# Kernel optimization log

Measured on AMD Instinct MI355X. Metric: run time of the kernel, lower is better.

## Reference

```python
import jax, jax.numpy as jnp
import numpy as np

EPS = 1e-08

def _compute_W(V, C, eps=EPS):
    # W = H_k ... H_1, applied sequentially as in the torch loop
    W = jnp.eye(C, dtype=V.dtype)
    def step(W, v):
        v = v / (jnp.linalg.norm(v) + eps)
        # H @ W = W - 2 v (v^T W)
        W = W - 2.0 * jnp.outer(v, v @ W)
        return W, None
    W, _ = jax.lax.scan(step, W, V)
    return W

def setup_inputs() -> dict:
    key = jax.random.key(0)
    k1, k2 = jax.random.split(key)
    x = jax.random.normal(k1, (16, 512, 64, 64), dtype=jnp.float32)
    V = jax.random.normal(k2, (32, 512), dtype=jnp.float32)
    return {"x": x, "V": V}

def reference(x, V):
    B, C, H, Wd = x.shape
    W = _compute_W(V, C)  # [C, C] orthogonal
    # 1x1 conv: out[b,o,h,w] = sum_c W[o,c] * x[b,c,h,w]
    return jnp.einsum('oc,bchw->bohw', W, x)
```

## Files before the change

### kernel.cpp

```cpp
#include <hip/hip_runtime.h>
#include <hip/hip_bf16.h>
#include <stdint.h>
#include <stddef.h>

#define HH_EPS 1e-8f

typedef __attribute__((ext_vector_type(8))) short short8;
typedef __attribute__((ext_vector_type(4))) float f32x4;

__global__ void normalize_v(const float* __restrict__ V, float* __restrict__ vhat) {
    const int k = blockIdx.x;
    const int lane = threadIdx.x;
    const float4* row = (const float4*)(V + (size_t)k * 512);
    float4 a = row[lane * 2 + 0];
    float4 b = row[lane * 2 + 1];
    float ss = a.x*a.x + a.y*a.y + a.z*a.z + a.w*a.w
             + b.x*b.x + b.y*b.y + b.z*b.z + b.w*b.w;
    #pragma unroll
    for (int off = 32; off > 0; off >>= 1) ss += __shfl_xor(ss, off);
    const float inv = 1.0f / (sqrtf(ss) + HH_EPS);
    float4* orow = (float4*)(vhat + (size_t)k * 512);
    orow[lane * 2 + 0] = make_float4(a.x*inv, a.y*inv, a.z*inv, a.w*inv);
    orow[lane * 2 + 1] = make_float4(b.x*inv, b.y*inv, b.z*inv, b.w*inv);
}

__global__ void compute_w(const float* __restrict__ vhat,
                          __hip_bfloat16* __restrict__ Wb) {
    const int wave = threadIdx.x >> 6;
    const int lane = threadIdx.x & 63;
    const int j = blockIdx.x * 4 + wave;
    const int ib = lane * 8;

    float w[8];
    #pragma unroll
    for (int r = 0; r < 8; r++) w[r] = (ib + r == j) ? 1.0f : 0.0f;

    for (int k = 0; k < 32; k++) {
        const float4* vp = (const float4*)(vhat + (size_t)k * 512 + ib);
        float4 v0 = vp[0], v1 = vp[1];
        float v[8] = {v0.x, v0.y, v0.z, v0.w, v1.x, v1.y, v1.z, v1.w};
        float d = 0.0f;
        #pragma unroll
        for (int r = 0; r < 8; r++) d += v[r] * w[r];
        #pragma unroll
        for (int off = 32; off > 0; off >>= 1) d += __shfl_xor(d, off);
        const float t = 2.0f * d;
        #pragma unroll
        for (int r = 0; r < 8; r++) w[r] -= t * v[r];
    }
    #pragma unroll
    for (int r = 0; r < 8; r++)
        Wb[(size_t)(ib + r) * 512 + j] = __float2bfloat16(w[r]);
}

#define BM 128
#define BN 128
#define BK 32
#define CDIM 512
#define SDIM 4096
#define BROW 40

__global__ __launch_bounds__(256, 2) void hh_gemm(
    const float* __restrict__ x,
    const __hip_bfloat16* __restrict__ Wb,
    float* __restrict__ out)
{
    __shared__ __attribute__((aligned(16))) __hip_bfloat16 Alds[BM * BK];
    __shared__ __attribute__((aligned(16))) __hip_bfloat16 Blds[BN * BROW];

    const int tid  = threadIdx.x;
    const int wave = tid >> 6, lane = tid & 63;
    const int quad = lane >> 4, l16 = lane & 15;
    const int wm = wave >> 1, wn = wave & 1;

    const int mt = blockIdx.x;
    const int nt = blockIdx.y;
    const int b  = blockIdx.z;
    const int m0 = mt * BM, n0 = nt * BN;

    const float* xb = x + (size_t)b * CDIM * SDIM;

    f32x4 acc[4][4];
    #pragma unroll
    for (int i = 0; i < 4; i++)
        #pragma unroll
        for (int jj = 0; jj < 4; jj++) {
            f32x4 z = {0.0f, 0.0f, 0.0f, 0.0f};
            acc[i][jj] = z;
        }

    for (int kt = 0; kt < CDIM / BK; kt++) {
        const int k0 = kt * BK;
        __syncthreads();

        #pragma unroll
        for (int c = 0; c < 2; c++) {
            const int chunk = c * 256 + tid;
            const int row = chunk >> 2, seg = chunk & 3;
            const short8 av = *(const short8*)(Wb + (size_t)(m0 + row) * CDIM + k0 + seg * 8);
            *(short8*)(&Alds[chunk * 8]) = av;
        }

        #pragma unroll
        for (int c = 0; c < 2; c++) {
            const int u = c * 256 + tid;
            const int n = u & 127, kg = u >> 7;
            const float* gp = xb + (size_t)(k0 + kg * 8) * SDIM + n0 + n;
            float f[8];
            #pragma unroll
            for (int jj = 0; jj < 8; jj++) f[jj] = gp[(size_t)jj * SDIM];
            short8 pk;
            #pragma unroll
            for (int jj = 0; jj < 8; jj++) {
                __hip_bfloat16 h = __float2bfloat16(f[jj]);
                pk[jj] = *(short*)&h;
            }
            *(short8*)(&Blds[n * BROW + kg * 8]) = pk;
        }
        __syncthreads();

        short8 af[4], bfr[4];
        #pragma unroll
        for (int mi = 0; mi < 4; mi++)
            af[mi] = *(const short8*)(&Alds[(wm * 64 + mi * 16 + l16) * BK + quad * 8]);
        #pragma unroll
        for (int ni = 0; ni < 4; ni++)
            bfr[ni] = *(const short8*)(&Blds[(wn * 64 + ni * 16 + l16) * BROW + quad * 8]);
        #pragma unroll
        for (int mi = 0; mi < 4; mi++)
            #pragma unroll
            for (int ni = 0; ni < 4; ni++)
                acc[mi][ni] = __builtin_amdgcn_mfma_f32_16x16x32_bf16(
                    af[mi], bfr[ni], acc[mi][ni], 0, 0, 0);
    }

    float* ob = out + (size_t)b * CDIM * SDIM;
    #pragma unroll
    for (int mi = 0; mi < 4; mi++) {
        #pragma unroll
        for (int ni = 0; ni < 4; ni++) {
            const int col = n0 + wn * 64 + ni * 16 + l16;
            #pragma unroll
            for (int r = 0; r < 4; r++) {
                const int row = m0 + wm * 64 + mi * 16 + quad * 4 + r;
                ob[(size_t)row * SDIM + col] = acc[mi][ni][r];
            }
        }
    }
}

extern "C" void kernel_launch(void* const* d_in, const int* in_sizes, int n_in,
                              void* d_out, int out_size, void* d_ws, size_t ws_size,
                              hipStream_t stream) {
    const float* x = (const float*)d_in[0];
    const float* V = (const float*)d_in[1];
    float* out = (float*)d_out;

    float* vhat = (float*)d_ws;
    __hip_bfloat16* Wb = (__hip_bfloat16*)((char*)d_ws + 65536);

    normalize_v<<<32, 64, 0, stream>>>(V, vhat);
    compute_w<<<128, 256, 0, stream>>>(vhat, Wb);
    dim3 grid(4, 32, 16);
    hh_gemm<<<grid, 256, 0, stream>>>(x, Wb, out);
}
```

Measured before the change: 287.6 us.

## Double-buffer GEMM tiles, fuse normalization into W build, remap grid

Folds the V normalization into compute_w: the squared norm is reduced alongside the dot products, and each wave now handles two columns of W, which removes one kernel launch and the vhat round trip. The GEMM gets double-buffered LDS with register prefetch of the next K tile, so global loads overlap the MFMA work and there is one barrier per iteration. It also uses a 1D grid ordered so consecutive blocks share the same M tile, and raises launch bounds to 3 blocks per CU. The costs are higher register and LDS use per block and a possible occupancy shortfall if the compiler cannot fit three blocks.

```diff
diff --git a/kernel.cpp b/kernel.cpp
--- a/kernel.cpp
+++ b/kernel.cpp
@@ -8,49 +8,57 @@
 typedef __attribute__((ext_vector_type(8))) short short8;
 typedef __attribute__((ext_vector_type(4))) float f32x4;
 
-__global__ void normalize_v(const float* __restrict__ V, float* __restrict__ vhat) {
-    const int k = blockIdx.x;
-    const int lane = threadIdx.x;
-    const float4* row = (const float4*)(V + (size_t)k * 512);
-    float4 a = row[lane * 2 + 0];
-    float4 b = row[lane * 2 + 1];
-    float ss = a.x*a.x + a.y*a.y + a.z*a.z + a.w*a.w
-             + b.x*b.x + b.y*b.y + b.z*b.z + b.w*b.w;
-    #pragma unroll
-    for (int off = 32; off > 0; off >>= 1) ss += __shfl_xor(ss, off);
-    const float inv = 1.0f / (sqrtf(ss) + HH_EPS);
-    float4* orow = (float4*)(vhat + (size_t)k * 512);
-    orow[lane * 2 + 0] = make_float4(a.x*inv, a.y*inv, a.z*inv, a.w*inv);
-    orow[lane * 2 + 1] = make_float4(b.x*inv, b.y*inv, b.z*inv, b.w*inv);
-}
-
-__global__ void compute_w(const float* __restrict__ vhat,
+__global__ void compute_w(const float* __restrict__ V,
                           __hip_bfloat16* __restrict__ Wb) {
     const int wave = threadIdx.x >> 6;
     const int lane = threadIdx.x & 63;
-    const int j = blockIdx.x * 4 + wave;
+    const int jA = (blockIdx.x * 4 + wave) * 2;
+    const int jB = jA + 1;
     const int ib = lane * 8;
 
-    float w[8];
-    #pragma unroll
-    for (int r = 0; r < 8; r++) w[r] = (ib + r == j) ? 1.0f : 0.0f;
+    float wA[8], wB[8];
+    #pragma unroll
+    for (int r = 0; r < 8; r++) {
+        wA[r] = (ib + r == jA) ? 1.0f : 0.0f;
+        wB[r] = (ib + r == jB) ? 1.0f : 0.0f;
+    }
+
+    float4 c0 = *(const float4*)(V + ib);
+    float4 c1 = *(const float4*)(V + ib + 4);
 
     for (int k = 0; k < 32; k++) {
-        const float4* vp = (const float4*)(vhat + (size_t)k * 512 + ib);
-        float4 v0 = vp[0], v1 = vp[1];
-        float v[8] = {v0.x, v0.y, v0.z, v0.w, v1.x, v1.y, v1.z, v1.w};
-        float d = 0.0f;
-        #pragma unroll
-        for (int r = 0; r < 8; r++) d += v[r] * w[r];
-        #pragma unroll
-        for (int off = 32; off > 0; off >>= 1) d += __shfl_xor(d, off);
-        const float t = 2.0f * d;
-        #pragma unroll
-        for (int r = 0; r < 8; r++) w[r] -= t * v[r];
-    }
-    #pragma unroll
-    for (int r = 0; r < 8; r++)
-        Wb[(size_t)(ib + r) * 512 + j] = __float2bfloat16(w[r]);
+        const float v[8] = {c0.x, c0.y, c0.z, c0.w, c1.x, c1.y, c1.z, c1.w};
+        if (k < 31) {
+            c0 = *(const float4*)(V + (size_t)(k + 1) * 512 + ib);
+            c1 = *(const float4*)(V + (size_t)(k + 1) * 512 + ib + 4);
+        }
+        float dA = 0.0f, dB = 0.0f, ss = 0.0f;
+        #pragma unroll
+        for (int r = 0; r < 8; r++) {
+            dA += v[r] * wA[r];
+            dB += v[r] * wB[r];
+            ss += v[r] * v[r];
+        }
+        #pragma unroll
+        for (int off = 32; off > 0; off >>= 1) {
+            dA += __shfl_xor(dA, off);
+            dB += __shfl_xor(dB, off);
+            ss += __shfl_xor(ss, off);
+        }
+        const float t = sqrtf(ss) + HH_EPS;
+        const float scale = 2.0f / (t * t);
+        const float tA = scale * dA, tB = scale * dB;
+        #pragma unroll
+        for (int r = 0; r < 8; r++) {
+            wA[r] -= tA * v[r];
+            wB[r] -= tB * v[r];
+        }
+    }
+    #pragma unroll
+    for (int r = 0; r < 8; r++) {
+        Wb[(size_t)(ib + r) * 512 + jA] = __float2bfloat16(wA[r]);
+        Wb[(size_t)(ib + r) * 512 + jB] = __float2bfloat16(wB[r]);
+    }
 }
 
 #define BM 128
@@ -60,22 +68,67 @@
 #define SDIM 4096
 #define BROW 40
 
-__global__ __launch_bounds__(256, 2) void hh_gemm(
+__device__ __forceinline__ void issue_loads(
+    const float* __restrict__ xb, const __hip_bfloat16* __restrict__ Wb,
+    int k0, int m0, int n0, int tid, short8 a_pf[2], float b_pf[16])
+{
+    #pragma unroll
+    for (int c = 0; c < 2; c++) {
+        const int chunk = c * 256 + tid;
+        const int row = chunk >> 2, seg = chunk & 3;
+        a_pf[c] = *(const short8*)(Wb + (size_t)(m0 + row) * CDIM + k0 + seg * 8);
+    }
+    #pragma unroll
+    for (int c = 0; c < 2; c++) {
+        const int u = c * 256 + tid;
+        const int n = u & 127, kg = u >> 7;
+        const float* gp = xb + (size_t)(k0 + kg * 8) * SDIM + n0 + n;
+        #pragma unroll
+        for (int j = 0; j < 8; j++) b_pf[c * 8 + j] = gp[(size_t)j * SDIM];
+    }
+}
+
+__device__ __forceinline__ void write_lds(
+    __hip_bfloat16* __restrict__ Al, __hip_bfloat16* __restrict__ Bl,
+    int tid, const short8 a_pf[2], const float b_pf[16])
+{
+    #pragma unroll
+    for (int c = 0; c < 2; c++) {
+        const int chunk = c * 256 + tid;
+        *(short8*)(&Al[chunk * 8]) = a_pf[c];
+    }
+    #pragma unroll
+    for (int c = 0; c < 2; c++) {
+        const int u = c * 256 + tid;
+        const int n = u & 127, kg = u >> 7;
+        short8 pk;
+        #pragma unroll
+        for (int j = 0; j < 8; j++) {
+            __hip_bfloat16 h = __float2bfloat16(b_pf[c * 8 + j]);
+            pk[j] = *(short*)&h;
+        }
+        *(short8*)(&Bl[n * BROW + kg * 8]) = pk;
+    }
+}
+
+__global__ __launch_bounds__(256, 3) void hh_gemm(
     const float* __restrict__ x,
     const __hip_bfloat16* __restrict__ Wb,
     float* __restrict__ out)
 {
-    __shared__ __attribute__((aligned(16))) __hip_bfloat16 Alds[BM * BK];
-    __shared__ __attribute__((aligned(16))) __hip_bfloat16 Blds[BN * BROW];
+    __shared__ __attribute__((aligned(16))) __hip_bfloat16 Alds[2][BM * BK];
+    __shared__ __attribute__((aligned(16))) __hip_bfloat16 Blds[2][BN * BROW];
 
     const int tid  = threadIdx.x;
     const int wave = tid >> 6, lane = tid & 63;
     const int quad = lane >> 4, l16 = lane & 15;
     const int wm = wave >> 1, wn = wave & 1;
 
-    const int mt = blockIdx.x;
-    const int nt = blockIdx.y;
-    const int b  = blockIdx.z;
+    const int bid  = blockIdx.x;
+    const int mt   = bid >> 9;
+    const int rest = bid & 511;
+    const int b    = rest >> 5;
+    const int nt   = rest & 31;
     const int m0 = mt * BM, n0 = nt * BN;
 
     const float* xb = x + (size_t)b * CDIM * SDIM;
@@ -89,49 +142,36 @@
             acc[i][jj] = z;
         }
 
+    short8 a_pf[2];
+    float  b_pf[16];
+
+    issue_loads(xb, Wb, 0, m0, n0, tid, a_pf, b_pf);
+    write_lds(Alds[0], Blds[0], tid, a_pf, b_pf);
+    __syncthreads();
+
     for (int kt = 0; kt < CDIM / BK; kt++) {
-        const int k0 = kt * BK;
-        __syncthreads();
-
-        #pragma unroll
-        for (int c = 0; c < 2; c++) {
-            const int chunk = c * 256 + tid;
-            const int row = chunk >> 2, seg = chunk & 3;
-            const short8 av = *(const short8*)(Wb + (size_t)(m0 + row) * CDIM + k0 + seg * 8);
-            *(short8*)(&Alds[chunk * 8]) = av;
-        }
-
-        #pragma unroll
-        for (int c = 0; c < 2; c++) {
-            const int u = c * 256 + tid;
-            const int n = u & 127, kg = u >> 7;
-            const float* gp = xb + (size_t)(k0 + kg * 8) * SDIM + n0 + n;
-            float f[8];
-            #pragma unroll
-            for (int jj = 0; jj < 8; jj++) f[jj] = gp[(size_t)jj * SDIM];
-            short8 pk;
-            #pragma unroll
-            for (int jj = 0; jj < 8; jj++) {
-                __hip_bfloat16 h = __float2bfloat16(f[jj]);
-                pk[jj] = *(short*)&h;
-            }
-            *(short8*)(&Blds[n * BROW + kg * 8]) = pk;
-        }
-        __syncthreads();
+        const int cur = kt & 1;
+
+        if (kt < CDIM / BK - 1)
+            issue_loads(xb, Wb, (kt + 1) * BK, m0, n0, tid, a_pf, b_pf);
 
         short8 af[4], bfr[4];
         #pragma unroll
         for (int mi = 0; mi < 4; mi++)
-            af[mi] = *(const short8*)(&Alds[(wm * 64 + mi * 16 + l16) * BK + quad * 8]);
+            af[mi] = *(const short8*)(&Alds[cur][(wm * 64 + mi * 16 + l16) * BK + quad * 8]);
         #pragma unroll
         for (int ni = 0; ni < 4; ni++)
-            bfr[ni] = *(const short8*)(&Blds[(wn * 64 + ni * 16 + l16) * BROW + quad * 8]);
+            bfr[ni] = *(const short8*)(&Blds[cur][(wn * 64 + ni * 16 + l16) * BROW + quad * 8]);
         #pragma unroll
         for (int mi = 0; mi < 4; mi++)
             #pragma unroll
             for (int ni = 0; ni < 4; ni++)
                 acc[mi][ni] = __builtin_amdgcn_mfma_f32_16x16x32_bf16(
                     af[mi], bfr[ni], acc[mi][ni], 0, 0, 0);
+
+        if (kt < CDIM / BK - 1)
+            write_lds(Alds[cur ^ 1], Blds[cur ^ 1], tid, a_pf, b_pf);
+        __syncthreads();
     }
 
     float* ob = out + (size_t)b * CDIM * SDIM;
@@ -156,11 +196,8 @@
     const float* V = (const float*)d_in[1];
     float* out = (float*)d_out;
 
-    float* vhat = (float*)d_ws;
-    __hip_bfloat16* Wb = (__hip_bfloat16*)((char*)d_ws + 65536);
-
-    normalize_v<<<32, 64, 0, stream>>>(V, vhat);
-    compute_w<<<128, 256, 0, stream>>>(vhat, Wb);
-    dim3 grid(4, 32, 16);
-    hh_gemm<<<grid, 256, 0, stream>>>(x, Wb, out);
-}
+    __hip_bfloat16* Wb = (__hip_bfloat16*)d_ws;
+
+    compute_w<<<64, 256, 0, stream>>>(V, Wb);
+    hh_gemm<<<2048, 256, 0, stream>>>(x, Wb, out);
+}
```

Result: slower. 299.1 us (+4.0%).
